# Performance work log

Measured on AMD Instinct MI355X. Metric: run time of the kernel, lower is better.

Reference implementation:

```python
import math
import jax, jax.numpy as jnp
import numpy as np

B, N, T, H = 4, 64, 384, 256
LAGS = (1, 5, 21)
L = len(LAGS)
NU = 500  # peer-universe size for rank buffers
TOPK = 8
LN_EPS = 1e-5


def setup_inputs() -> dict:
    key = jax.random.key(0)
    ks = jax.random.split(key, 24)
    s = 1.0 / np.sqrt(H)

    def lin(i):
        w = jax.random.uniform(ks[i], (H, H), jnp.float32, -s, s)
        b = jax.random.uniform(ks[i + 1], (H,), jnp.float32, -s, s)
        return w, b

    wq_w, wq_b = lin(0)
    wk_w, wk_b = lin(2)
    wv_w, wv_b = lin(4)
    f1_w, f1_b = lin(6)
    f2_w, f2_b = lin(8)
    return dict(
        target_h=jax.random.normal(ks[10], (B, T, H), jnp.float32),
        peer_h=jax.random.normal(ks[11], (B, N, T, H), jnp.float32),
        wq_w=wq_w, wq_b=wq_b, wk_w=wk_w, wk_b=wk_b, wv_w=wv_w, wv_b=wv_b,
        f1_w=f1_w, f1_b=f1_b, f2_w=f2_w, f2_b=f2_b,
        ln_g=jnp.ones((H,), jnp.float32),
        ln_b=jnp.zeros((H,), jnp.float32),
        alpha=jnp.float32(0.1),
        log_rank_strength=jnp.log(jnp.clip(jax.random.uniform(ks[12], (L, NU, NU)), 1e-6, None)),
        peer_mask=jnp.ones((B, N), dtype=bool),
        rank_topk_mask=jax.random.uniform(ks[13], (L, NU, NU)) < 0.2,
        target_id=jax.random.randint(ks[14], (B,), 0, NU),
        peer_id=jax.random.randint(ks[15], (B, N), 0, NU),
    )


def _forward(target_h, peer_h, wq_w, wq_b, wk_w, wk_b, wv_w, wv_b,
             f1_w, f1_b, f2_w, f2_b, ln_g, ln_b, alpha, log_rank_strength,
             peer_mask, rank_topk_mask, target_id, peer_id):
    lags = jnp.array(LAGS, dtype=jnp.int32)
    t_idx = jnp.arange(T, dtype=jnp.int32)[None, :] - lags[:, None]   # [L,T]
    valid_time = t_idx >= 0                                           # [L,T]
    t_idx_c = jnp.maximum(t_idx, 0)

    # lag-gathered peer features: [B,N,L,T,H] -> [B,T,N,L,H]
    peer_h_lag = jnp.transpose(peer_h[:, :, t_idx_c, :], (0, 3, 1, 2, 4))

    Q = target_h @ wq_w.T + wq_b                  # [B,T,H]
    K = peer_h_lag @ wk_w.T + wk_b                # [B,T,N,L,H]
    # delta-valued V path (use_delta_value=True): current minus lagged
    peer_h_now = jnp.transpose(peer_h, (0, 2, 1, 3))[:, :, :, None, :]  # [B,T,N,1,H]
    V = (peer_h_now - peer_h_lag) @ wv_w.T + wv_b  # [B,T,N,L,H]

    logits = jnp.einsum('bth,btnlh->btnl', Q, K) / math.sqrt(H)  # [B,T,N,L]

    # Bennett soft bias (use_bennett=True)
    tgt_b = jnp.broadcast_to(target_id[:, None], (B, N))          # [B,N]
    prior = jnp.transpose(log_rank_strength[:, peer_id, tgt_b], (1, 2, 0))  # [B,N,L]
    logits = logits + alpha * prior[:, None, :, :]

    neg_inf = jnp.float32(-jnp.inf)
    logits = jnp.where(valid_time.T[None, :, None, :], logits, neg_inf)      # time validity
    logits = jnp.where(peer_mask[:, None, :, None], logits, neg_inf)         # peer mask
    rmask = jnp.transpose(rank_topk_mask[:, peer_id, tgt_b], (1, 2, 0))      # [B,N,L]
    logits = jnp.where(rmask[:, None, :, :], logits, neg_inf)                # hard rank mask

    NL = N * L
    k = min(TOPK, NL)
    logits_flat = logits.reshape(B, T, NL)
    topk_vals, topk_idx = jax.lax.top_k(logits_flat, k)            # [B,T,k]
    is_inf = jnp.isinf(topk_vals)
    all_inf = jnp.all(is_inf, axis=-1, keepdims=True)
    topk_safe = jnp.where(is_inf, jnp.float32(-1e9), topk_vals)
    weights = jax.nn.softmax(topk_safe, axis=-1)
    weights = weights * (~all_inf).astype(weights.dtype)

    V_flat = V.reshape(B, T, NL, H)
    V_sel = jnp.take_along_axis(V_flat, topk_idx[..., None], axis=2)  # [B,T,k,H]
    ll_y = jnp.sum(weights[..., None] * V_sel, axis=2)                # [B,T,H]

    ffn = jax.nn.elu(ll_y @ f1_w.T + f1_b) @ f2_w.T + f2_b
    x = ll_y + ffn
    mu = jnp.mean(x, axis=-1, keepdims=True)
    var = jnp.var(x, axis=-1, keepdims=True)
    return (x - mu) / jnp.sqrt(var + LN_EPS) * ln_g + ln_b


def reference(target_h, peer_h, wq_w, wq_b, wk_w, wk_b, wv_w, wv_b,
              f1_w, f1_b, f2_w, f2_b, ln_g, ln_b, alpha, log_rank_strength,
              peer_mask, rank_topk_mask, target_id, peer_id):
    return _forward(target_h, peer_h, wq_w, wq_b, wk_w, wk_b, wv_w, wv_b,
                    f1_w, f1_b, f2_w, f2_b, ln_g, ln_b, alpha, log_rank_strength,
                    peer_mask, rank_topk_mask, target_id, peer_id)
```

## Files before the change

kernel.cpp:

```cpp
#include <hip/hip_runtime.h>
#include <hip/hip_bf16.h>


#define NU_ 500

__device__ __forceinline__ bool mask_at(const void* p, long i, int mode){
  if (mode == 1) return ((const unsigned char*)p)[i] != 0;
  if (mode == 2) return ((const unsigned short*)p)[i] != 0;
  return ((const unsigned int*)p)[i] != 0;
}
__device__ __forceinline__ int lag_of(int l){ return (l == 0) ? 1 : ((l == 1) ? 5 : 21); }

__global__ __launch_bounds__(256) void qproj_prep_kernel(
    const float* __restrict__ xg, const float* __restrict__ wq, const float* __restrict__ wqb,
    const float* __restrict__ wk, const float* __restrict__ wkb,
    const float* __restrict__ lrs, const void* __restrict__ pmask, const void* __restrict__ rmask,
    const int* __restrict__ target_id, const int* __restrict__ peer_id,
    const float* __restrict__ alpha_p,
    float* __restrict__ Qt, float* __restrict__ qb, float* __restrict__ prior)
{
  if (blockIdx.x >= 192){
    const int b = blockIdx.x - 192;
    const int c = threadIdx.x;
    if (c >= 192) return;
    const unsigned char* pmB = (const unsigned char*)pmask;
    const unsigned char p0 = pmB[0], p1 = pmB[1];
    int mmode;
    if (p0 == 0x01u)      mmode = (p1 == 0x01u) ? 1 : 0;
    else if (p0 == 0x80u) mmode = 2;
    else                  mmode = 0;
    const int n = c / 3, l = c - n * 3;
    const int pid = peer_id[b * 64 + n];
    const int tgt = target_id[b];
    const long ridx = (long)l * (NU_*NU_) + (long)pid * NU_ + tgt;
    const bool ok = mask_at(pmask, b * 64 + n, mmode) && mask_at(rmask, ridx, mmode);
    prior[b * 192 + c] = ok ? alpha_p[0] * lrs[ridx] : -__builtin_inff();
    return;
  }
  __shared__ __align__(16) float xs[8][256];
  __shared__ __align__(16) float qs[8][256];
  const int j = threadIdx.x;
  const int row0 = blockIdx.x * 8;
  #pragma unroll
  for (int r = 0; r < 8; ++r) xs[r][j] = xg[(long)(row0 + r) * 256 + j];
  __syncthreads();

  float acc[8];
  #pragma unroll
  for (int r = 0; r < 8; ++r) acc[r] = 0.f;
  const float4* wrow = (const float4*)(wq + (long)j * 256);
  for (int h8 = 0; h8 < 32; ++h8){
    float4 wa = wrow[h8 * 2], wb = wrow[h8 * 2 + 1];
    const int h = h8 * 8;
    #pragma unroll
    for (int r = 0; r < 8; ++r){
      const float* xr = &xs[r][h];
      acc[r] += xr[0]*wa.x + xr[1]*wa.y + xr[2]*wa.z + xr[3]*wa.w
              + xr[4]*wb.x + xr[5]*wb.y + xr[6]*wb.z + xr[7]*wb.w;
    }
  }
  const float bq = wqb[j];
  #pragma unroll
  for (int r = 0; r < 8; ++r) qs[r][j] = acc[r] + bq;
  __syncthreads();

  float at[8];
  #pragma unroll
  for (int r = 0; r < 8; ++r) at[r] = 0.f;
  for (int h = 0; h < 256; ++h){
    const float w = wk[(long)h * 256 + j];
    #pragma unroll
    for (int r = 0; r < 8; ++r) at[r] += qs[r][h] * w;
  }
  #pragma unroll
  for (int r = 0; r < 8; ++r) Qt[(long)(row0 + r) * 256 + j] = at[r];

  const float bk = wkb[j];
  #pragma unroll
  for (int r = 0; r < 8; ++r) xs[r][j] = qs[r][j] * bk;
  __syncthreads();
  if (j < 8){
    float s = 0.f;
    for (int h = 0; h < 256; ++h) s += xs[j][h];
    qb[row0 + j] = s;
  }
}

__global__ __launch_bounds__(256) void attn_kernel(
    const float* __restrict__ peer_h, const float* __restrict__ Qt,
    const float* __restrict__ qbv, const float* __restrict__ prior,
    float* __restrict__ dvec, float* __restrict__ ssum)
{
  __shared__ __align__(16) float qt_s[256];
  __shared__ float pr_s[192];
  __shared__ float lg[192];
  __shared__ int   ix_s[192];
  __shared__ int   wcnt[4];
  __shared__ int   seli[8];
  __shared__ float selw[8];
  __shared__ int   allinf_sh;
  const int bt = blockIdx.x;
  const int b = bt / 384, t = bt % 384;
  const int tid = threadIdx.x;
  const int lane = tid & 63, wvi = tid >> 6;
  const float NEG_INF = -__builtin_inff();

  qt_s[tid] = Qt[(long)bt * 256 + tid];
  bool valid = false;
  if (tid < 192){
    pr_s[tid] = prior[b * 192 + tid];
    lg[tid] = NEG_INF;
    ix_s[tid] = 1000 + tid;
    const int l = tid - (tid / 3) * 3;
    valid = (t >= lag_of(l)) && (pr_s[tid] > -3.0e38f);
  }
  const unsigned long long bal = __ballot(valid);
  if (lane == 0) wcnt[wvi] = __popcll(bal);
  __syncthreads();
  const int cnt = wcnt[0] + wcnt[1] + wcnt[2];
  if (valid){
    int base = 0;
    for (int i = 0; i < wvi; ++i) base += wcnt[i];
    const int pos = base + __popcll(bal & ((1ULL << lane) - 1ULL));
    ix_s[pos] = tid;
  }
  __syncthreads();

  const float qb = qbv[bt];
  const int group = tid >> 4, q = tid & 15;
  float qv[16];
  #pragma unroll
  for (int i = 0; i < 4; ++i){
    float4 f = *(const float4*)&qt_s[q * 16 + i * 4];
    qv[i*4] = f.x; qv[i*4+1] = f.y; qv[i*4+2] = f.z; qv[i*4+3] = f.w;
  }

  for (int i = group; i < cnt; i += 16){
    const int c = ix_s[i];
    const int n = c / 3, l = c - n * 3;
    const int tc = t - lag_of(l);
    const float4* rp = (const float4*)(peer_h + (((long)(b*64 + n)) * 384 + tc) * 256);
    float4 u0 = rp[q*4], u1 = rp[q*4+1], u2 = rp[q*4+2], u3 = rp[q*4+3];
    float p = u0.x*qv[0] + u0.y*qv[1] + u0.z*qv[2] + u0.w*qv[3]
            + u1.x*qv[4] + u1.y*qv[5] + u1.z*qv[6] + u1.w*qv[7]
            + u2.x*qv[8] + u2.y*qv[9] + u2.z*qv[10]+ u2.w*qv[11]
            + u3.x*qv[12]+ u3.y*qv[13]+ u3.z*qv[14]+ u3.w*qv[15];
    #pragma unroll
    for (int off = 1; off < 16; off <<= 1) p += __shfl_xor(p, off);
    if (q == 0) lg[i] = (p + qb) * 0.0625f + pr_s[c];
  }
  __syncthreads();

  if (tid < 64){
    float v0 = lg[lane], v1 = lg[lane + 64], v2 = lg[lane + 128];
    int   i0 = ix_s[lane], i1 = ix_s[lane + 64], i2 = ix_s[lane + 128];
    float sv[8]; int si[8];
    for (int k = 0; k < 8; ++k){
      float mv = v0; int mi = i0; int ms = 0;
      if (v1 > mv || (v1 == mv && i1 < mi)){ mv = v1; mi = i1; ms = 1; }
      if (v2 > mv || (v2 == mv && i2 < mi)){ mv = v2; mi = i2; ms = 2; }
      #pragma unroll
      for (int off = 32; off; off >>= 1){
        float ov = __shfl_xor(mv, off);
        int   oi = __shfl_xor(mi, off);
        int   os = __shfl_xor(ms, off);
        if (ov > mv || (ov == mv && oi < mi)){ mv = ov; mi = oi; ms = os; }
      }
      sv[k] = mv; si[k] = mi;
      if (mi == i0 && ms == 0)      v0 = NEG_INF;
      else if (mi == i1 && ms == 1) v1 = NEG_INF;
      else if (mi == i2 && ms == 2) v2 = NEG_INF;
    }
    const int allinf = (sv[0] == NEG_INF) ? 1 : 0;
    const float m = allinf ? -1e9f : sv[0];
    float e[8]; float tot = 0.f;
    #pragma unroll
    for (int k = 0; k < 8; ++k){
      const float s = (sv[k] == NEG_INF) ? -1e9f : sv[k];
      e[k] = expf(s - m);
      tot += e[k];
    }
    if (lane == 0){
      allinf_sh = allinf;
      const float inv = 1.f / tot;
      for (int k = 0; k < 8; ++k){
        seli[k] = si[k];
        selw[k] = allinf ? 0.f : e[k] * inv;
      }
    }
  }
  __syncthreads();

  float acc = 0.f;
  const int h = tid;
  #pragma unroll
  for (int k = 0; k < 8; ++k){
    const float w = selw[k];
    const int c = min(seli[k], 191);
    const int n = c / 3, l = c - n * 3;
    const int tc = max(t - lag_of(l), 0);
    const long base = ((long)(b*64 + n)) * 384;
    acc += w * (peer_h[(base + t ) * 256 + h]
              - peer_h[(base + tc) * 256 + h]);
  }
  dvec[(long)bt * 256 + h] = acc;
  if (tid == 0) ssum[bt] = allinf_sh ? 0.f : 1.f;
}

__global__ __launch_bounds__(256) void ffn_kernel(
    const float* __restrict__ dv, const float* __restrict__ sv,
    const float* __restrict__ wv, const float* __restrict__ wvb,
    const float* __restrict__ f1, const float* __restrict__ f1b,
    const float* __restrict__ f2, const float* __restrict__ f2b,
    const float* __restrict__ lng, const float* __restrict__ lnb,
    float* __restrict__ out)
{
  __shared__ __align__(16) float ds[8][256];
  __shared__ __align__(16) float ys[8][256];
  __shared__ float mu_s[8], rs_s[8];
  const int j = threadIdx.x;
  const int row0 = blockIdx.x * 8;
  #pragma unroll
  for (int r = 0; r < 8; ++r) ds[r][j] = dv[(long)(row0 + r) * 256 + j];
  __syncthreads();

  float ll[8];
  {
    #pragma unroll
    for (int r = 0; r < 8; ++r) ll[r] = 0.f;
    const float4* wrow = (const float4*)(wv + (long)j * 256);
    for (int h8 = 0; h8 < 32; ++h8){
      float4 wa = wrow[h8 * 2], wb = wrow[h8 * 2 + 1];
      const int h = h8 * 8;
      #pragma unroll
      for (int r = 0; r < 8; ++r){
        const float* xr = &ds[r][h];
        ll[r] += xr[0]*wa.x + xr[1]*wa.y + xr[2]*wa.z + xr[3]*wa.w
               + xr[4]*wb.x + xr[5]*wb.y + xr[6]*wb.z + xr[7]*wb.w;
      }
    }
    const float bv = wvb[j];
    #pragma unroll
    for (int r = 0; r < 8; ++r) ll[r] += sv[row0 + r] * bv;
  }
  #pragma unroll
  for (int r = 0; r < 8; ++r) ys[r][j] = ll[r];
  __syncthreads();

  {
    float a[8];
    #pragma unroll
    for (int r = 0; r < 8; ++r) a[r] = 0.f;
    const float4* wrow = (const float4*)(f1 + (long)j * 256);
    for (int h8 = 0; h8 < 32; ++h8){
      float4 wa = wrow[h8 * 2], wb = wrow[h8 * 2 + 1];
      const int h = h8 * 8;
      #pragma unroll
      for (int r = 0; r < 8; ++r){
        const float* xr = &ys[r][h];
        a[r] += xr[0]*wa.x + xr[1]*wa.y + xr[2]*wa.z + xr[3]*wa.w
              + xr[4]*wb.x + xr[5]*wb.y + xr[6]*wb.z + xr[7]*wb.w;
      }
    }
    const float b1 = f1b[j];
    #pragma unroll
    for (int r = 0; r < 8; ++r){
      const float x = a[r] + b1;
      ds[r][j] = (x > 0.f) ? x : expm1f(x);
    }
  }
  __syncthreads();

  float xv[8];
  {
    float a[8];
    #pragma unroll
    for (int r = 0; r < 8; ++r) a[r] = 0.f;
    const float4* wrow = (const float4*)(f2 + (long)j * 256);
    for (int h8 = 0; h8 < 32; ++h8){
      float4 wa = wrow[h8 * 2], wb = wrow[h8 * 2 + 1];
      const int h = h8 * 8;
      #pragma unroll
      for (int r = 0; r < 8; ++r){
        const float* xr = &ds[r][h];
        a[r] += xr[0]*wa.x + xr[1]*wa.y + xr[2]*wa.z + xr[3]*wa.w
              + xr[4]*wb.x + xr[5]*wb.y + xr[6]*wb.z + xr[7]*wb.w;
      }
    }
    const float b2_ = f2b[j];
    #pragma unroll
    for (int r = 0; r < 8; ++r) xv[r] = ll[r] + a[r] + b2_;
  }
  #pragma unroll
  for (int r = 0; r < 8; ++r) ys[r][j] = xv[r];
  __syncthreads();

  {
    const int lane = j & 63, wvi = j >> 6;
    for (int rr = 0; rr < 2; ++rr){
      const int r = wvi * 2 + rr;
      float s = 0.f, qq = 0.f;
      for (int p = lane; p < 256; p += 64){ const float x = ys[r][p]; s += x; qq += x * x; }
      #pragma unroll
      for (int off = 32; off; off >>= 1){ s += __shfl_xor(s, off); qq += __shfl_xor(qq, off); }
      if (lane == 0){
        const float mu = s * (1.f/256.f);
        const float var = qq * (1.f/256.f) - mu * mu;
        mu_s[r] = mu; rs_s[r] = rsqrtf(var + 1e-5f);
      }
    }
  }
  __syncthreads();
  const float gj = lng[j], bj = lnb[j];
  #pragma unroll
  for (int r = 0; r < 8; ++r){
    const float o = (ys[r][j] - mu_s[r]) * rs_s[r] * gj + bj;
    out[(long)(row0 + r) * 256 + j] = o;
  }
}

extern "C" void kernel_launch(void* const* d_in, const int* in_sizes, int n_in,
                              void* d_out, int out_size, void* d_ws, size_t ws_size,
                              hipStream_t stream)
{
  (void)in_sizes; (void)n_in; (void)out_size; (void)ws_size;
  const float* target_h = (const float*)d_in[0];
  const float* peer_h   = (const float*)d_in[1];
  const float* wq_w = (const float*)d_in[2];  const float* wq_b = (const float*)d_in[3];
  const float* wk_w = (const float*)d_in[4];  const float* wk_b = (const float*)d_in[5];
  const float* wv_w = (const float*)d_in[6];  const float* wv_b = (const float*)d_in[7];
  const float* f1_w = (const float*)d_in[8];  const float* f1_b = (const float*)d_in[9];
  const float* f2_w = (const float*)d_in[10]; const float* f2_b = (const float*)d_in[11];
  const float* ln_g = (const float*)d_in[12]; const float* ln_b = (const float*)d_in[13];
  const float* alpha = (const float*)d_in[14];
  const float* lrs  = (const float*)d_in[15];
  const void* pmask = d_in[16];
  const void* rmask = d_in[17];
  const int* target_id = (const int*)d_in[18];
  const int* peer_id   = (const int*)d_in[19];

  float* prior = (float*)d_ws;
  float* Qt    = prior + 4 * 192;
  float* qb    = Qt + 393216;
  float* dvec  = qb + 1536;
  float* ssum  = dvec + 393216;

  qproj_prep_kernel<<<196, 256, 0, stream>>>(target_h, wq_w, wq_b, wk_w, wk_b,
      lrs, pmask, rmask, target_id, peer_id, alpha, Qt, qb, prior);
  attn_kernel<<<1536, 256, 0, stream>>>(peer_h, Qt, qb, prior, dvec, ssum);
  ffn_kernel<<<192, 256, 0, stream>>>(dvec, ssum, wv_w, wv_b, f1_w, f1_b,
                                      f2_w, f2_b, ln_g, ln_b, (float*)d_out);
}
```

Measured before the change: 263.8 us.

## Halve rows per block, vectorise LDS reads, widen attention dot-product per thread

The projection and FFN kernels now handle 4 rows per block instead of 8, doubling the grid so more CUs are busy, and they read activations from shared memory as float4. The qb bias reduction is parallelised across waves with shuffles instead of running on 8 serial threads. The attention logit loop gives each thread 32 elements (8 lanes per candidate) and pads the shared Q vector to avoid bank conflicts, so fewer shuffle steps are needed. The cost is higher register pressure and that each weight load is now reused across fewer rows.

Measured after the change: 281.8 us. 1.07x slower.

```diff
diff --git a/kernel.cpp b/kernel.cpp
--- a/kernel.cpp
+++ b/kernel.cpp
@@ -10,6 +10,9 @@
   return ((const unsigned int*)p)[i] != 0;
 }
 __device__ __forceinline__ int lag_of(int l){ return (l == 0) ? 1 : ((l == 1) ? 5 : 21); }
+__device__ __forceinline__ float fsel(float4 v, int c){
+  return (c == 0) ? v.x : (c == 1) ? v.y : (c == 2) ? v.z : v.w;
+}
 
 __global__ __launch_bounds__(256) void qproj_prep_kernel(
     const float* __restrict__ xg, const float* __restrict__ wq, const float* __restrict__ wqb,
@@ -19,8 +22,8 @@
     const float* __restrict__ alpha_p,
     float* __restrict__ Qt, float* __restrict__ qb, float* __restrict__ prior)
 {
-  if (blockIdx.x >= 192){
-    const int b = blockIdx.x - 192;
+  if (blockIdx.x >= 384){
+    const int b = blockIdx.x - 384;
     const int c = threadIdx.x;
     if (c >= 192) return;
     const unsigned char* pmB = (const unsigned char*)pmask;
@@ -37,52 +40,58 @@
     prior[b * 192 + c] = ok ? alpha_p[0] * lrs[ridx] : -__builtin_inff();
     return;
   }
-  __shared__ __align__(16) float xs[8][256];
-  __shared__ __align__(16) float qs[8][256];
+  __shared__ __align__(16) float xs[4][256];
+  __shared__ __align__(16) float qs[4][256];
   const int j = threadIdx.x;
-  const int row0 = blockIdx.x * 8;
-  #pragma unroll
-  for (int r = 0; r < 8; ++r) xs[r][j] = xg[(long)(row0 + r) * 256 + j];
-  __syncthreads();
-
-  float acc[8];
-  #pragma unroll
-  for (int r = 0; r < 8; ++r) acc[r] = 0.f;
+  const int lane = j & 63, wvi = j >> 6;
+  const int row0 = blockIdx.x * 4;
+  #pragma unroll
+  for (int r = 0; r < 4; ++r) xs[r][j] = xg[(long)(row0 + r) * 256 + j];
+  __syncthreads();
+
+  float acc[4] = {0.f, 0.f, 0.f, 0.f};
   const float4* wrow = (const float4*)(wq + (long)j * 256);
   for (int h8 = 0; h8 < 32; ++h8){
     float4 wa = wrow[h8 * 2], wb = wrow[h8 * 2 + 1];
     const int h = h8 * 8;
     #pragma unroll
-    for (int r = 0; r < 8; ++r){
-      const float* xr = &xs[r][h];
-      acc[r] += xr[0]*wa.x + xr[1]*wa.y + xr[2]*wa.z + xr[3]*wa.w
-              + xr[4]*wb.x + xr[5]*wb.y + xr[6]*wb.z + xr[7]*wb.w;
+    for (int r = 0; r < 4; ++r){
+      float4 xa = *(const float4*)&xs[r][h];
+      float4 xb = *(const float4*)&xs[r][h + 4];
+      acc[r] += xa.x*wa.x + xa.y*wa.y + xa.z*wa.z + xa.w*wa.w
+              + xb.x*wb.x + xb.y*wb.y + xb.z*wb.z + xb.w*wb.w;
     }
   }
   const float bq = wqb[j];
   #pragma unroll
-  for (int r = 0; r < 8; ++r) qs[r][j] = acc[r] + bq;
-  __syncthreads();
-
-  float at[8];
-  #pragma unroll
-  for (int r = 0; r < 8; ++r) at[r] = 0.f;
-  for (int h = 0; h < 256; ++h){
-    const float w = wk[(long)h * 256 + j];
-    #pragma unroll
-    for (int r = 0; r < 8; ++r) at[r] += qs[r][h] * w;
-  }
-  #pragma unroll
-  for (int r = 0; r < 8; ++r) Qt[(long)(row0 + r) * 256 + j] = at[r];
-
-  const float bk = wkb[j];
-  #pragma unroll
-  for (int r = 0; r < 8; ++r) xs[r][j] = qs[r][j] * bk;
-  __syncthreads();
-  if (j < 8){
+  for (int r = 0; r < 4; ++r) qs[r][j] = acc[r] + bq;
+  __syncthreads();
+
+  float at[4] = {0.f, 0.f, 0.f, 0.f};
+  for (int h4 = 0; h4 < 64; ++h4){
+    const int h = h4 * 4;
+    float4 q0 = *(const float4*)&qs[0][h];
+    float4 q1 = *(const float4*)&qs[1][h];
+    float4 q2 = *(const float4*)&qs[2][h];
+    float4 q3 = *(const float4*)&qs[3][h];
+    #pragma unroll
+    for (int c = 0; c < 4; ++c){
+      const float w = wk[(long)(h + c) * 256 + j];
+      at[0] += fsel(q0, c) * w;
+      at[1] += fsel(q1, c) * w;
+      at[2] += fsel(q2, c) * w;
+      at[3] += fsel(q3, c) * w;
+    }
+  }
+  #pragma unroll
+  for (int r = 0; r < 4; ++r) Qt[(long)(row0 + r) * 256 + j] = at[r];
+
+  {
     float s = 0.f;
-    for (int h = 0; h < 256; ++h) s += xs[j][h];
-    qb[row0 + j] = s;
+    for (int p = lane; p < 256; p += 64) s += qs[wvi][p] * wkb[p];
+    #pragma unroll
+    for (int off = 32; off; off >>= 1) s += __shfl_xor(s, off);
+    if (lane == 0) qb[row0 + wvi] = s;
   }
 }
 
@@ -91,7 +100,7 @@
     const float* __restrict__ qbv, const float* __restrict__ prior,
     float* __restrict__ dvec, float* __restrict__ ssum)
 {
-  __shared__ __align__(16) float qt_s[256];
+  __shared__ __align__(16) float qt_s[288];
   __shared__ float pr_s[192];
   __shared__ float lg[192];
   __shared__ int   ix_s[192];
@@ -105,7 +114,7 @@
   const int lane = tid & 63, wvi = tid >> 6;
   const float NEG_INF = -__builtin_inff();
 
-  qt_s[tid] = Qt[(long)bt * 256 + tid];
+  qt_s[tid + ((tid >> 5) << 2)] = Qt[(long)bt * 256 + tid];
   bool valid = false;
   if (tid < 192){
     pr_s[tid] = prior[b * 192 + tid];
@@ -127,26 +136,27 @@
   __syncthreads();
 
   const float qb = qbv[bt];
-  const int group = tid >> 4, q = tid & 15;
-  float qv[16];
-  #pragma unroll
-  for (int i = 0; i < 4; ++i){
-    float4 f = *(const float4*)&qt_s[q * 16 + i * 4];
-    qv[i*4] = f.x; qv[i*4+1] = f.y; qv[i*4+2] = f.z; qv[i*4+3] = f.w;
-  }
-
-  for (int i = group; i < cnt; i += 16){
+  const int group = tid >> 3, q = tid & 7;
+  float qv[32];
+  #pragma unroll
+  for (int k = 0; k < 8; ++k){
+    float4 f = *(const float4*)&qt_s[36 * q + 4 * k];
+    qv[4*k] = f.x; qv[4*k+1] = f.y; qv[4*k+2] = f.z; qv[4*k+3] = f.w;
+  }
+
+  for (int i = group; i < cnt; i += 32){
     const int c = ix_s[i];
     const int n = c / 3, l = c - n * 3;
     const int tc = t - lag_of(l);
     const float4* rp = (const float4*)(peer_h + (((long)(b*64 + n)) * 384 + tc) * 256);
-    float4 u0 = rp[q*4], u1 = rp[q*4+1], u2 = rp[q*4+2], u3 = rp[q*4+3];
-    float p = u0.x*qv[0] + u0.y*qv[1] + u0.z*qv[2] + u0.w*qv[3]
-            + u1.x*qv[4] + u1.y*qv[5] + u1.z*qv[6] + u1.w*qv[7]
-            + u2.x*qv[8] + u2.y*qv[9] + u2.z*qv[10]+ u2.w*qv[11]
-            + u3.x*qv[12]+ u3.y*qv[13]+ u3.z*qv[14]+ u3.w*qv[15];
-    #pragma unroll
-    for (int off = 1; off < 16; off <<= 1) p += __shfl_xor(p, off);
+    float p = 0.f;
+    #pragma unroll
+    for (int k = 0; k < 8; ++k){
+      float4 u = rp[q * 8 + k];
+      p += u.x*qv[4*k] + u.y*qv[4*k+1] + u.z*qv[4*k+2] + u.w*qv[4*k+3];
+    }
+    #pragma unroll
+    for (int off = 1; off < 8; off <<= 1) p += __shfl_xor(p, off);
     if (q == 0) lg[i] = (p + qb) * 0.0625f + pr_s[c];
   }
   __syncthreads();
@@ -215,105 +225,101 @@
     const float* __restrict__ lng, const float* __restrict__ lnb,
     float* __restrict__ out)
 {
-  __shared__ __align__(16) float ds[8][256];
-  __shared__ __align__(16) float ys[8][256];
-  __shared__ float mu_s[8], rs_s[8];
+  __shared__ __align__(16) float ds[4][256];
+  __shared__ __align__(16) float ys[4][256];
+  __shared__ float mu_s[4], rs_s[4];
   const int j = threadIdx.x;
-  const int row0 = blockIdx.x * 8;
-  #pragma unroll
-  for (int r = 0; r < 8; ++r) ds[r][j] = dv[(long)(row0 + r) * 256 + j];
-  __syncthreads();
-
-  float ll[8];
-  {
-    #pragma unroll
-    for (int r = 0; r < 8; ++r) ll[r] = 0.f;
+  const int lane = j & 63, wvi = j >> 6;
+  const int row0 = blockIdx.x * 4;
+  #pragma unroll
+  for (int r = 0; r < 4; ++r) ds[r][j] = dv[(long)(row0 + r) * 256 + j];
+  __syncthreads();
+
+  float ll[4] = {0.f, 0.f, 0.f, 0.f};
+  {
     const float4* wrow = (const float4*)(wv + (long)j * 256);
     for (int h8 = 0; h8 < 32; ++h8){
       float4 wa = wrow[h8 * 2], wb = wrow[h8 * 2 + 1];
       const int h = h8 * 8;
       #pragma unroll
-      for (int r = 0; r < 8; ++r){
-        const float* xr = &ds[r][h];
-        ll[r] += xr[0]*wa.x + xr[1]*wa.y + xr[2]*wa.z + xr[3]*wa.w
-               + xr[4]*wb.x + xr[5]*wb.y + xr[6]*wb.z + xr[7]*wb.w;
+      for (int r = 0; r < 4; ++r){
+        float4 xa = *(const float4*)&ds[r][h];
+        float4 xb = *(const float4*)&ds[r][h + 4];
+        ll[r] += xa.x*wa.x + xa.y*wa.y + xa.z*wa.z + xa.w*wa.w
+               + xb.x*wb.x + xb.y*wb.y + xb.z*wb.z + xb.w*wb.w;
       }
     }
     const float bv = wvb[j];
     #pragma unroll
-    for (int r = 0; r < 8; ++r) ll[r] += sv[row0 + r] * bv;
-  }
-  #pragma unroll
-  for (int r = 0; r < 8; ++r) ys[r][j] = ll[r];
-  __syncthreads();
-
-  {
-    float a[8];
-    #pragma unroll
-    for (int r = 0; r < 8; ++r) a[r] = 0.f;
+    for (int r = 0; r < 4; ++r) ll[r] += sv[row0 + r] * bv;
+  }
+  #pragma unroll
+  for (int r = 0; r < 4; ++r) ys[r][j] = ll[r];
+  __syncthreads();
+
+  {
+    float a[4] = {0.f, 0.f, 0.f, 0.f};
     const float4* wrow = (const float4*)(f1 + (long)j * 256);
     for (int h8 = 0; h8 < 32; ++h8){
       float4 wa = wrow[h8 * 2], wb = wrow[h8 * 2 + 1];
       const int h = h8 * 8;
       #pragma unroll
-      for (int r = 0; r < 8; ++r){
-        const float* xr = &ys[r][h];
-        a[r] += xr[0]*wa.x + xr[1]*wa.y + xr[2]*wa.z + xr[3]*wa.w
-              + xr[4]*wb.x + xr[5]*wb.y + xr[6]*wb.z + xr[7]*wb.w;
+      for (int r = 0; r < 4; ++r){
+        float4 xa = *(const float4*)&ys[r][h];
+        float4 xb = *(const float4*)&ys[r][h + 4];
+        a[r] += xa.x*wa.x + xa.y*wa.y + xa.z*wa.z + xa.w*wa.w
+              + xb.x*wb.x + xb.y*wb.y + xb.z*wb.z + xb.w*wb.w;
       }
     }
     const float b1 = f1b[j];
-    #pragma unroll
-    for (int r = 0; r < 8; ++r){
+    __syncthreads();
+    #pragma unroll
+    for (int r = 0; r < 4; ++r){
       const float x = a[r] + b1;
       ds[r][j] = (x > 0.f) ? x : expm1f(x);
     }
   }
   __syncthreads();
 
-  float xv[8];
-  {
-    float a[8];
-    #pragma unroll
-    for (int r = 0; r < 8; ++r) a[r] = 0.f;
+  float xv[4];
+  {
+    float a[4] = {0.f, 0.f, 0.f, 0.f};
     const float4* wrow = (const float4*)(f2 + (long)j * 256);
     for (int h8 = 0; h8 < 32; ++h8){
       float4 wa = wrow[h8 * 2], wb = wrow[h8 * 2 + 1];
       const int h = h8 * 8;
       #pragma unroll
-      for (int r = 0; r < 8; ++r){
-        const float* xr = &ds[r][h];
-        a[r] += xr[0]*wa.x + xr[1]*wa.y + xr[2]*wa.z + xr[3]*wa.w
-              + xr[4]*wb.x + xr[5]*wb.y + xr[6]*wb.z + xr[7]*wb.w;
+      for (int r = 0; r < 4; ++r){
+        float4 xa = *(const float4*)&ds[r][h];
+        float4 xb = *(const float4*)&ds[r][h + 4];
+        a[r] += xa.x*wa.x + xa.y*wa.y + xa.z*wa.z + xa.w*wa.w
+              + xb.x*wb.x + xb.y*wb.y + xb.z*wb.z + xb.w*wb.w;
       }
     }
     const float b2_ = f2b[j];
     #pragma unroll
-    for (int r = 0; r < 8; ++r) xv[r] = ll[r] + a[r] + b2_;
-  }
-  #pragma unroll
-  for (int r = 0; r < 8; ++r) ys[r][j] = xv[r];
-  __syncthreads();
-
-  {
-    const int lane = j & 63, wvi = j >> 6;
-    for (int rr = 0; rr < 2; ++rr){
-      const int r = wvi * 2 + rr;
-      float s = 0.f, qq = 0.f;
-      for (int p = lane; p < 256; p += 64){ const float x = ys[r][p]; s += x; qq += x * x; }
-      #pragma unroll
-      for (int off = 32; off; off >>= 1){ s += __shfl_xor(s, off); qq += __shfl_xor(qq, off); }
-      if (lane == 0){
-        const float mu = s * (1.f/256.f);
-        const float var = qq * (1.f/256.f) - mu * mu;
-        mu_s[r] = mu; rs_s[r] = rsqrtf(var + 1e-5f);
-      }
+    for (int r = 0; r < 4; ++r) xv[r] = ll[r] + a[r] + b2_;
+  }
+  __syncthreads();
+  #pragma unroll
+  for (int r = 0; r < 4; ++r) ys[r][j] = xv[r];
+  __syncthreads();
+
+  {
+    float s = 0.f, qq = 0.f;
+    for (int p = lane; p < 256; p += 64){ const float x = ys[wvi][p]; s += x; qq += x * x; }
+    #pragma unroll
+    for (int off = 32; off; off >>= 1){ s += __shfl_xor(s, off); qq += __shfl_xor(qq, off); }
+    if (lane == 0){
+      const float mu = s * (1.f/256.f);
+      const float var = qq * (1.f/256.f) - mu * mu;
+      mu_s[wvi] = mu; rs_s[wvi] = rsqrtf(var + 1e-5f);
     }
   }
   __syncthreads();
   const float gj = lng[j], bj = lnb[j];
   #pragma unroll
-  for (int r = 0; r < 8; ++r){
+  for (int r = 0; r < 4; ++r){
     const float o = (ys[r][j] - mu_s[r]) * rs_s[r] * gj + bj;
     out[(long)(row0 + r) * 256 + j] = o;
   }
@@ -345,9 +351,9 @@
   float* dvec  = qb + 1536;
   float* ssum  = dvec + 393216;
 
-  qproj_prep_kernel<<<196, 256, 0, stream>>>(target_h, wq_w, wq_b, wk_w, wk_b,
+  qproj_prep_kernel<<<388, 256, 0, stream>>>(target_h, wq_w, wq_b, wk_w, wk_b,
       lrs, pmask, rmask, target_id, peer_id, alpha, Qt, qb, prior);
   attn_kernel<<<1536, 256, 0, stream>>>(peer_h, Qt, qb, prior, dvec, ssum);
-  ffn_kernel<<<192, 256, 0, stream>>>(dvec, ssum, wv_w, wv_b, f1_w, f1_b,
+  ffn_kernel<<<384, 256, 0, stream>>>(dvec, ssum, wv_w, wv_b, f1_w, f1_b,
                                       f2_w, f2_b, ln_g, ln_b, (float*)d_out);
 }
```
